# Kernel tuning notes

Hardware: AMD Instinct MI355X
Metric: run time of the kernel (lower is better)

Reference implementation:

```python
import jax, jax.numpy as jnp
import numpy as np

E = 8            # num_experts
K = 2            # top-k
CF = 1.25        # capacity_factor
NOISE_STD = 1.0 / E   # noise_mult / num_experts


def setup_inputs() -> dict:
    key = jax.random.key(0)
    ks = jax.random.split(key, 4)
    B, S, D, H = 8, 1024, 768, 3072
    x = jax.random.normal(ks[0], (B, S, D), jnp.float32)
    router_w = jax.random.normal(ks[1], (D, E), jnp.float32) * 0.02
    fc1_w = jax.random.normal(ks[2], (E, D, H), jnp.float32) * 0.02
    fc1_b = jnp.zeros((E, H), jnp.float32)
    fc2_w = jax.random.normal(ks[3], (E, H, D), jnp.float32) * 0.02
    fc2_b = jnp.zeros((E, D), jnp.float32)
    return dict(x=x, router_w=router_w, fc1_w=fc1_w, fc1_b=fc1_b, fc2_w=fc2_w, fc2_b=fc2_b)


def reference(x, router_w, fc1_w, fc1_b, fc2_w, fc2_b):
    B, S, D = x.shape
    N = B * S
    A = N * K                                   # total (token, slot) assignments
    capacity = int(round(K * N * CF / E))
    x_flat = x.reshape(N, D)

    # ---- router (eval mode: no noise, no dropout) ----
    logits = (x_flat @ router_w).astype(jnp.float32)          # [N,E]
    clean_probs = jax.nn.softmax(logits, axis=-1)
    noisy_logits = logits
    noisy_probs = jax.nn.softmax(noisy_logits, axis=-1)
    topk_probs, topk_idx = jax.lax.top_k(noisy_probs, K)      # [N,K]
    topk_probs = topk_probs.astype(x.dtype)

    flat_e = topk_idx.reshape(-1)                             # [A]
    expert_counts = jax.ops.segment_sum(jnp.ones((A,), jnp.float32), flat_e, num_segments=E)

    # ---- aux losses ----
    importance = clean_probs.sum(0)
    mi = importance.mean()
    loss_importance = jnp.var(importance) / (mi * mi + 1e-6)
    # kthvalue(noisy_logits, E-K+1) == (E-K+1)-th smallest == sorted[:, E-K]
    threshold = jnp.sort(noisy_logits, axis=-1)[:, E - K][:, None]
    prob_selected = 1.0 - jax.scipy.stats.norm.cdf(threshold - logits, loc=0.0, scale=NOISE_STD)
    load = prob_selected.sum(0)
    ml = load.mean()
    loss_load = jnp.var(load) / (ml * ml + 1e-6)
    aux_loss = 0.5 * (loss_importance + loss_load)

    # ---- priority-based capacity dropping (vectorized over all assignments) ----
    priority = clean_probs.max(-1)                            # [N]
    tok = jnp.repeat(jnp.arange(N, dtype=jnp.int32), K)       # [A] token of each assignment
    kslot = jnp.tile(jnp.arange(K, dtype=jnp.int32), N)       # [A] which top-k slot
    score = priority[tok] - kslot.astype(jnp.float32)         # combined_scores = -k_idx + priority
    # group by expert (ascending), within expert sort by score descending
    sort_key = flat_e.astype(jnp.float32) * (K + 2) - score
    order = jnp.argsort(sort_key)
    e_sorted = flat_e[order]
    counts = jax.ops.segment_sum(jnp.ones((A,), jnp.int32), flat_e, num_segments=E)
    starts = jnp.cumsum(counts) - counts
    rank_sorted = jnp.arange(A, dtype=jnp.int32) - starts[e_sorted]   # position within expert group
    rank = jnp.zeros((A,), jnp.int32).at[order].set(rank_sorted)
    keep = rank < capacity
    dropped = jnp.sum(~keep).astype(jnp.int32)

    # ---- dispatch into fixed [E, capacity] buffer (overflow slot sliced off) ----
    pos = jnp.where(keep, flat_e * capacity + rank, E * capacity)
    dispatch_tok = jnp.zeros((E * capacity + 1,), jnp.int32).at[pos].set(tok)[:-1]
    w_flat = topk_probs.reshape(-1)
    weight_buf = jnp.zeros((E * capacity + 1,), x.dtype).at[pos].set(jnp.where(keep, w_flat, 0.0))[:-1]

    xe = x_flat[dispatch_tok].reshape(E, capacity, D)         # gather
    h = jax.nn.gelu(jnp.einsum('ecd,edh->ech', xe, fc1_w) + fc1_b[:, None, :], approximate=False)
    ye = jnp.einsum('ech,ehd->ecd', h, fc2_w) + fc2_b[:, None, :]
    weighted = ye * weight_buf.reshape(E, capacity, 1)
    # padded slots have weight 0 and token 0 -> contribute nothing
    out_flat = jnp.zeros((N, D), x.dtype).at[dispatch_tok].add(weighted.reshape(E * capacity, D))

    return out_flat.reshape(B, S, D), aux_loss, dropped, expert_counts
```

## Files before the change

### kernel.cpp

```cpp
#include <hip/hip_runtime.h>
#include <hip/hip_bf16.h>
#include <math.h>

#define NTOK 8192
#define DIM  768
#define HDIM 3072
#define NE   8
#define CAP  2560
#define AMAX 16384

typedef __bf16 bf16x8  __attribute__((ext_vector_type(8)));
typedef __bf16 bf16x2  __attribute__((ext_vector_type(2)));
typedef float  floatx4 __attribute__((ext_vector_type(4)));

typedef unsigned int u32_g __attribute__((address_space(1)));
typedef unsigned int u32_l __attribute__((address_space(3)));

__device__ __forceinline__ void gl_lds16(const void* g, void* l) {
  __builtin_amdgcn_global_load_lds((const u32_g*)g, (u32_l*)l, 16, 0, 0);
}

__device__ __forceinline__ float gelu_exact(float v) {
  float z = fabsf(v) * 0.7071067811865475f;
  float t = __builtin_amdgcn_rcpf(1.0f + 0.3275911f * z);
  float p = ((((1.061405429f * t - 1.453152027f) * t + 1.421413741f) * t
              - 0.284496736f) * t + 0.254829592f) * t;
  float e = 1.0f - p * __expf(-z * z);
  e = copysignf(e, v);
  return 0.5f * v * (1.0f + e);
}

__global__ __launch_bounds__(256) void transpose_conv2(
    const float* __restrict__ w1, const float* __restrict__ w2,
    __bf16* __restrict__ o1, __bf16* __restrict__ o2)
{
  const int which = blockIdx.z;
  const float* src = which ? w2 : w1;
  __bf16* dst = which ? o2 : o1;
  const int Kd = which ? HDIM : DIM;
  const int Nd = which ? DIM : HDIM;
  const int e = blockIdx.y;
  const int tilesK = Kd >> 6;
  const int bk = blockIdx.x % tilesK, bn = blockIdx.x / tilesK;
  __shared__ float T[64][65];
  const float* se = src + (size_t)e * Kd * Nd;
  const int k0 = bk * 64, n0 = bn * 64;
  const int tid = threadIdx.x;
#pragma unroll
  for (int it = 0; it < 16; ++it) {
    int flat = tid + it * 256;
    int kk = flat >> 6, nn = flat & 63;
    T[kk][nn] = se[(size_t)(k0 + kk) * Nd + n0 + nn];
  }
  __syncthreads();
  const int n = tid >> 2, kg = tid & 3;
  bf16x8 v0, v1;
#pragma unroll
  for (int q = 0; q < 8; ++q) v0[q] = (__bf16)T[kg * 16 + q][n];
#pragma unroll
  for (int q = 0; q < 8; ++q) v1[q] = (__bf16)T[kg * 16 + 8 + q][n];
  __bf16* de = dst + (size_t)e * Nd * Kd + (size_t)(n0 + n) * Kd + k0 + kg * 16;
  *(bf16x8*)(de) = v0;
  *(bf16x8*)(de + 8) = v1;
}

__global__ __launch_bounds__(256) void router_kernel(
    const float* __restrict__ x, const float* __restrict__ rw,
    int* __restrict__ list_len, double* __restrict__ imp, double* __restrict__ loadacc,
    int* __restrict__ aidx, float* __restrict__ keyarr, float* __restrict__ warr)
{
  __shared__ float Wl[NE * DIM];
  __shared__ int   lcount[NE], lbase[NE];
  __shared__ int   s_e[32][2], s_pos[32][2];
  __shared__ float s_key[32][2], s_w[32][2];
  const int tid = threadIdx.x;
  for (int i = tid; i < NE * DIM; i += 256) {
    int e = i / DIM, d = i - e * DIM;
    Wl[i] = rw[d * NE + e];
  }
  if (tid < NE) lcount[tid] = 0;
  __syncthreads();
  const int wave = tid >> 6, lane = tid & 63;
  double my_imp = 0.0, my_load = 0.0;

  for (int it = 0; it < 8; ++it) {
    const int t = wave * 8 + it;
    const int n = blockIdx.x * 32 + t;
    const float* xr = x + (size_t)n * DIM;
    float part[NE];
#pragma unroll
    for (int e = 0; e < NE; ++e) part[e] = 0.f;
#pragma unroll
    for (int c = 0; c < DIM / 64; ++c) {
      float xv = xr[c * 64 + lane];
#pragma unroll
      for (int e = 0; e < NE; ++e) part[e] += xv * Wl[e * DIM + c * 64 + lane];
    }
#pragma unroll
    for (int off = 32; off > 0; off >>= 1) {
#pragma unroll
      for (int e = 0; e < NE; ++e) part[e] += __shfl_xor(part[e], off);
    }
    int e0 = 0; float v0 = part[0];
#pragma unroll
    for (int e = 1; e < NE; ++e) if (part[e] > v0) { v0 = part[e]; e0 = e; }
    int e1 = -1; float v1 = -3.4e38f;
#pragma unroll
    for (int e = 0; e < NE; ++e) if (e != e0 && part[e] > v1) { v1 = part[e]; e1 = e; }

    float pexp[NE]; float s = 0.f;
#pragma unroll
    for (int e = 0; e < NE; ++e) { pexp[e] = expf(part[e] - v0); s += pexp[e]; }
    const float inv = 1.0f / s;
    const float pr = inv;
    float w1v = 0.f;
#pragma unroll
    for (int e = 0; e < NE; ++e) if (e == e1) w1v = pexp[e] * inv;

    float myl = 0.f, mypexp = 0.f;
#pragma unroll
    for (int e = 0; e < NE; ++e) if (lane == e) { myl = part[e]; mypexp = pexp[e]; }
    if (lane < NE) {
      my_imp  += (double)(mypexp * inv);
      my_load += (double)(0.5f * erfcf((v1 - myl) * 5.656854249492380f));
    }
    if (lane == 0) {
      int p0 = atomicAdd(&lcount[e0], 1);
      int p1 = atomicAdd(&lcount[e1], 1);
      s_e[t][0] = e0; s_pos[t][0] = p0;
      s_key[t][0] = (float)(e0 * 4) - pr;
      s_w[t][0] = pr;
      s_e[t][1] = e1; s_pos[t][1] = p1;
      s_key[t][1] = (float)(e1 * 4) - (pr - 1.0f);
      s_w[t][1] = w1v;
    }
  }
  __syncthreads();
  if (tid < NE) lbase[tid] = atomicAdd(&list_len[tid], lcount[tid]);
  __syncthreads();
  if (tid < 64) {
    const int t = tid >> 1, sl = tid & 1;
    const int e = s_e[t][sl];
    const int gp = lbase[e] + s_pos[t][sl];
    const int n = blockIdx.x * 32 + t;
    aidx[e * AMAX + gp]   = n * 2 + sl;
    keyarr[e * AMAX + gp] = s_key[t][sl];
    warr[e * AMAX + gp]   = s_w[t][sl];
  }
  if (lane < NE) {
    unsafeAtomicAdd(&imp[lane], my_imp);
    unsafeAtomicAdd(&loadacc[lane], my_load);
  }
}

__global__ __launch_bounds__(256) void compact_kernel(
    const int* __restrict__ list_len, const int* __restrict__ aidx,
    const float* __restrict__ keyarr, const float* __restrict__ warr,
    int* __restrict__ dtok, float* __restrict__ dw,
    const double* __restrict__ imp, const double* __restrict__ loadacc,
    float* __restrict__ out_scalars)
{
  __shared__ float sk[6144];
  __shared__ int   sa[6144];
  const int e = blockIdx.x, tid = threadIdx.x;
  const int C = list_len[e];
  if (C <= CAP) {
    for (int t = tid; t < C; t += 256) {
      int a = aidx[e * AMAX + t];
      dtok[e * CAP + t] = a >> 1;
      dw[e * CAP + t]   = warr[e * AMAX + t];
    }
  } else {
    const bool useL = (C <= 6144);
    if (useL) {
      for (int t = tid; t < C; t += 256) { sk[t] = keyarr[e*AMAX+t]; sa[t] = aidx[e*AMAX+t]; }
      __syncthreads();
    }
    for (int t = tid; t < C; t += 256) {
      float kt = keyarr[e*AMAX+t]; int at = aidx[e*AMAX+t];
      int r = 0;
      for (int u = 0; u < C; ++u) {
        float ku = useL ? sk[u] : keyarr[e*AMAX+u];
        int   au = useL ? sa[u] : aidx[e*AMAX+u];
        if (ku < kt || (ku == kt && au < at)) ++r;
      }
      if (r < CAP) { dtok[e*CAP + r] = at >> 1; dw[e*CAP + r] = warr[e*AMAX+t]; }
    }
  }
  if (e == 0 && tid == 0) {
    double mi = 0, ml = 0;
    for (int i = 0; i < NE; ++i) { mi += imp[i]; ml += loadacc[i]; }
    mi /= NE; ml /= NE;
    double vi = 0, vl = 0;
    for (int i = 0; i < NE; ++i) {
      double di = imp[i] - mi;     vi += di * di;
      double dl = loadacc[i] - ml; vl += dl * dl;
    }
    vi /= NE; vl /= NE;
    double li = vi / (mi * mi + 1e-6), ll = vl / (ml * ml + 1e-6);
    out_scalars[0] = (float)(0.5 * (li + ll));
    int drop = 0;
    for (int i = 0; i < NE; ++i) { int c2 = list_len[i]; if (c2 > CAP) drop += c2 - CAP; }
    out_scalars[1] = (float)drop;
    for (int i = 0; i < NE; ++i) out_scalars[2 + i] = (float)list_len[i];
  }
}

__global__ __launch_bounds__(256) void gather_kernel(
    const float* __restrict__ x, const int* __restrict__ dtok,
    const int* __restrict__ list_len, __bf16* __restrict__ Ag)
{
  const int row  = blockIdx.x * 4 + (threadIdx.x >> 6);
  const int lane = threadIdx.x & 63;
  const int e = row / CAP, slot = row - e * CAP;
  const int kept = min(list_len[e], CAP);
  __bf16* dst = Ag + (size_t)row * DIM;
  if (slot < kept) {
    const float* srcr = x + (size_t)dtok[e * CAP + slot] * DIM;
#pragma unroll
    for (int c = 0; c < DIM / 128; ++c) {
      float2 v = *(const float2*)(srcr + c * 128 + lane * 2);
      bf16x2 o; o[0] = (__bf16)v.x; o[1] = (__bf16)v.y;
      *(bf16x2*)(dst + c * 128 + lane * 2) = o;
    }
  } else {
    bf16x2 z; z[0] = (__bf16)0.f; z[1] = (__bf16)0.f;
#pragma unroll
    for (int c = 0; c < DIM / 128; ++c) *(bf16x2*)(dst + c * 128 + lane * 2) = z;
  }
}

template<int MODE>
__global__ __launch_bounds__(256, 2) void moe_gemm(
    const __bf16* __restrict__ Aall, const __bf16* __restrict__ BTall,
    const float* __restrict__ bias, __bf16* __restrict__ Hout,
    float* __restrict__ Out, const int* __restrict__ dtok, const float* __restrict__ dww,
    const int* __restrict__ list_len, int Kd, int Nd, int tilesM)
{
  const int i_blk = blockIdx.x;
  const int xcd = i_blk & 7, q = i_blk >> 3;
  const int e = xcd;
  const int tm = q % tilesM;
  int tn, ks, kbase, kIters;
  if (MODE == 0) {
    tn = q / tilesM; ks = 0; kbase = 0; kIters = Kd >> 5;
  } else {
    const int pr = q / tilesM;
    tn = pr % 3; ks = pr / 3; kbase = ks * (Kd >> 1); kIters = Kd >> 6;
  }

  const int kept = min(list_len[e], CAP);
  const int mUsed = (kept + 127) >> 7;
  if (tm >= mUsed) return;

  __shared__ __bf16 S[3][12288];

  const int tid = threadIdx.x, lane = tid & 63, wave = tid >> 6;
  const int wm = wave & 1, wn = wave >> 1;
  const int m0 = tm * 128, n0 = tn * 256;

  const __bf16* Ae = Aall + (size_t)e * CAP * Kd + kbase;
  const __bf16* Be = BTall + (size_t)e * Nd * Kd + kbase;

  const int lr = lane & 15, lc = (lane >> 4) * 8;
  const __bf16* gA[2]; const __bf16* gB[4];
  int sAo[2], sBo[4];
#pragma unroll
  for (int a = 0; a < 2; ++a) {
    const int g = wave * 2 + a;
    gA[a] = Ae + (size_t)(m0 + g * 16 + lr) * Kd + lc;
    sAo[a] = g * 512;
  }
#pragma unroll
  for (int b = 0; b < 4; ++b) {
    const int h = wave * 4 + b;
    gB[b] = Be + (size_t)(n0 + h * 16 + lr) * Kd + lc;
    sBo[b] = 4096 + h * 512;
  }

  floatx4 acc[4][8];
#pragma unroll
  for (int i = 0; i < 4; ++i)
#pragma unroll
    for (int j = 0; j < 8; ++j) acc[i][j] = (floatx4)0.f;

#define ISSUE(J, Bf)                                           \
  do {                                                         \
    const int _off = (J) * 32;                                 \
    gl_lds16(gA[0] + _off, &S[(Bf)][sAo[0]]);                  \
    gl_lds16(gA[1] + _off, &S[(Bf)][sAo[1]]);                  \
    gl_lds16(gB[0] + _off, &S[(Bf)][sBo[0]]);                  \
    gl_lds16(gB[1] + _off, &S[(Bf)][sBo[1]]);                  \
    gl_lds16(gB[2] + _off, &S[(Bf)][sBo[2]]);                  \
    gl_lds16(gB[3] + _off, &S[(Bf)][sBo[3]]);                  \
  } while (0)

  ISSUE(0, 0);
  ISSUE(1, 1);
  int cur = 0;
  for (int kt = 0; kt < kIters; ++kt) {
    if (kt < kIters - 1) __builtin_amdgcn_s_waitcnt(0x0F76);
    else                 __builtin_amdgcn_s_waitcnt(0x0F70);
    asm volatile("" ::: "memory");
    __builtin_amdgcn_s_barrier();
    asm volatile("" ::: "memory");

    bf16x8 af[4], bfr[8];
#pragma unroll
    for (int i = 0; i < 4; ++i)
      af[i]  = *(const bf16x8*)(&S[cur][((wm * 4 + i) * 64 + lane) * 8]);
#pragma unroll
    for (int j = 0; j < 8; ++j)
      bfr[j] = *(const bf16x8*)(&S[cur][4096 + ((wn * 8 + j) * 64 + lane) * 8]);

    if (kt + 2 < kIters) {
      int nb = cur + 2; if (nb >= 3) nb -= 3;
      ISSUE(kt + 2, nb);
    }

#pragma unroll
    for (int i = 0; i < 4; ++i)
#pragma unroll
      for (int j = 0; j < 8; ++j)
        acc[i][j] = __builtin_amdgcn_mfma_f32_16x16x32_bf16(af[i], bfr[j], acc[i][j], 0, 0, 0);

    cur = (cur == 2) ? 0 : cur + 1;
  }
#undef ISSUE

  const int quad = lane >> 4, lcol = lane & 15;
  float bcol[8];
#pragma unroll
  for (int j = 0; j < 8; ++j)
    bcol[j] = (MODE == 1 && ks == 1) ? 0.f : bias[e * Nd + n0 + wn * 128 + j * 16 + lcol];

  if (MODE == 0) {
#pragma unroll
    for (int i = 0; i < 4; ++i) {
#pragma unroll
      for (int r = 0; r < 4; ++r) {
        const int row = m0 + wm * 64 + i * 16 + quad * 4 + r;
        __bf16* hrow = Hout + ((size_t)(e * CAP + row)) * Nd;
#pragma unroll
        for (int j = 0; j < 8; ++j) {
          float v = acc[i][j][r] + bcol[j];
          hrow[n0 + wn * 128 + j * 16 + lcol] = (__bf16)gelu_exact(v);
        }
      }
    }
  } else {
#pragma unroll
    for (int i = 0; i < 4; ++i) {
#pragma unroll
      for (int r = 0; r < 4; ++r) {
        const int row = m0 + wm * 64 + i * 16 + quad * 4 + r;
        const float w = dww[e * CAP + row];
        if (w != 0.0f) {
          const int tok = dtok[e * CAP + row];
          float* orow = Out + (size_t)tok * DIM;
#pragma unroll
          for (int j = 0; j < 8; ++j) {
            float v = w * (acc[i][j][r] + bcol[j]);
            unsafeAtomicAdd(&orow[n0 + wn * 128 + j * 16 + lcol], v);
          }
        }
      }
    }
  }
}

extern "C" void kernel_launch(void* const* d_in, const int* in_sizes, int n_in,
                              void* d_out, int out_size, void* d_ws, size_t ws_size,
                              hipStream_t stream) {
  (void)in_sizes; (void)n_in; (void)out_size; (void)ws_size;
  const float* x  = (const float*)d_in[0];
  const float* rw = (const float*)d_in[1];
  const float* w1 = (const float*)d_in[2];
  const float* b1 = (const float*)d_in[3];
  const float* w2 = (const float*)d_in[4];
  const float* b2 = (const float*)d_in[5];
  float* out = (float*)d_out;
  char* ws = (char*)d_ws;

  int*    list_len = (int*)(ws + 0);
  double* imp      = (double*)(ws + 64);
  double* loadacc  = (double*)(ws + 128);
  int*    dtok     = (int*)(ws + 256);
  float*  dw       = (float*)(ws + 256 + 81920);
  int*    aidx     = (int*)(ws + 164096);
  float*  keyarr   = (float*)(ws + 164096 + 524288);
  float*  warr     = (float*)(ws + 164096 + 1048576);
  __bf16* W1T      = (__bf16*)(ws + 2097152);
  __bf16* W2T      = (__bf16*)(ws + 2097152 + 37748736);
  __bf16* Ag       = (__bf16*)(ws + 2097152 + 2 * 37748736);
  __bf16* hbuf     = (__bf16*)(ws + 2097152 + 2 * 37748736 + 31457280);

  hipMemsetAsync(d_out, 0, (size_t)NTOK * DIM * sizeof(float), stream);
  hipMemsetAsync(ws, 0, 164096, stream);

  transpose_conv2<<<dim3(576, 8, 2), 256, 0, stream>>>(w1, w2, W1T, W2T);
  router_kernel<<<NTOK / 32, 256, 0, stream>>>(x, rw, list_len, imp, loadacc, aidx, keyarr, warr);
  compact_kernel<<<NE, 256, 0, stream>>>(list_len, aidx, keyarr, warr, dtok, dw, imp, loadacc,
                                         out + (size_t)NTOK * DIM);
  gather_kernel<<<(NE * CAP) / 4, 256, 0, stream>>>(x, dtok, list_len, Ag);
  moe_gemm<0><<<NE * 20 * (HDIM / 256), 256, 0, stream>>>(
      Ag, W1T, b1, hbuf, nullptr, nullptr, nullptr, list_len, DIM, HDIM, 20);
  moe_gemm<1><<<NE * 20 * (DIM / 256) * 2, 256, 0, stream>>>(
      hbuf, W2T, b2, nullptr, out, dtok, dw, list_len, HDIM, DIM, 20);
}
```

Before: 577.8 us.

## Restructure MoE GEMMs into 256x256 tiles with 8-wave ping-pong pipeline

Replaces the 128x256 tile, 4-wave, triple-buffered GEMM with a 256x256 tile, 8-wave (512-thread) kernel. It uses two 64-wide K stages in LDS and interleaves quarter-tile LDS reads, global-to-LDS loads and MFMA blocks, separated by barriers and s_setprio. The second GEMM drops its split-K in favour of the full K loop, which halves its atomic adds but launches fewer blocks. The goal is higher arithmetic intensity per block and better overlap of loads with MFMA. The cost is 128 KB of LDS per block, more barriers, and less parallelism for the small-N second GEMM.

Result: faster. 549.0 us (-5.0%).

```diff
diff --git a/kernel.cpp b/kernel.cpp
--- a/kernel.cpp
+++ b/kernel.cpp
@@ -230,144 +230,185 @@
   }
 }
 
+#define BAR() do { asm volatile("" ::: "memory"); __builtin_amdgcn_s_barrier(); asm volatile("" ::: "memory"); } while (0)
+
+#define ST_A(h, t, buf) do { \
+    const __bf16* _g = gA[h] + (size_t)(t) * 64; \
+    gl_lds16(_g,      &S[buf][((h) * 8 + wave) * 1024]); \
+    gl_lds16(_g + 32, &S[buf][((h) * 8 + wave) * 1024 + 512]); \
+  } while (0)
+
+#define ST_B(h, t, buf) do { \
+    const __bf16* _g = gB[h] + (size_t)(t) * 64; \
+    gl_lds16(_g,      &S[buf][16384 + ((h) * 8 + wave) * 1024]); \
+    gl_lds16(_g + 32, &S[buf][16384 + ((h) * 8 + wave) * 1024 + 512]); \
+  } while (0)
+
+#define RD_A(qm, buf) do { \
+    _Pragma("unroll") \
+    for (int _m = 0; _m < 4; ++_m) { \
+      const int _g = wm * 8 + (qm) * 4 + _m; \
+      aR[_m][0] = *(const bf16x8*)&S[buf][(_g * 2 + 0) * 512 + lane * 8]; \
+      aR[_m][1] = *(const bf16x8*)&S[buf][(_g * 2 + 1) * 512 + lane * 8]; \
+    } \
+  } while (0)
+
+#define RD_B(qn, buf) do { \
+    _Pragma("unroll") \
+    for (int _n = 0; _n < 2; ++_n) { \
+      const int _g = wn * 4 + (qn) * 2 + _n; \
+      bR[(qn) * 2 + _n][0] = *(const bf16x8*)&S[buf][16384 + (_g * 2 + 0) * 512 + lane * 8]; \
+      bR[(qn) * 2 + _n][1] = *(const bf16x8*)&S[buf][16384 + (_g * 2 + 1) * 512 + lane * 8]; \
+    } \
+  } while (0)
+
+#define MM(qm, qn) do { \
+    __builtin_amdgcn_s_setprio(1); \
+    _Pragma("unroll") \
+    for (int _m = 0; _m < 4; ++_m) \
+      _Pragma("unroll") \
+      for (int _n = 0; _n < 2; ++_n) { \
+        acc[(qm) * 4 + _m][(qn) * 2 + _n] = __builtin_amdgcn_mfma_f32_16x16x32_bf16( \
+            aR[_m][0], bR[(qn) * 2 + _n][0], acc[(qm) * 4 + _m][(qn) * 2 + _n], 0, 0, 0); \
+        acc[(qm) * 4 + _m][(qn) * 2 + _n] = __builtin_amdgcn_mfma_f32_16x16x32_bf16( \
+            aR[_m][1], bR[(qn) * 2 + _n][1], acc[(qm) * 4 + _m][(qn) * 2 + _n], 0, 0, 0); \
+      } \
+    __builtin_amdgcn_s_setprio(0); \
+  } while (0)
+
 template<int MODE>
-__global__ __launch_bounds__(256, 2) void moe_gemm(
+__global__ __launch_bounds__(512, 2) void moe_gemm8(
     const __bf16* __restrict__ Aall, const __bf16* __restrict__ BTall,
     const float* __restrict__ bias, __bf16* __restrict__ Hout,
     float* __restrict__ Out, const int* __restrict__ dtok, const float* __restrict__ dww,
-    const int* __restrict__ list_len, int Kd, int Nd, int tilesM)
+    const int* __restrict__ list_len)
 {
+  const int Kd = MODE ? HDIM : DIM;
+  const int Nd = MODE ? DIM : HDIM;
+  const int numKt = Kd / 64;
+  const int nIter = numKt / 2;
+
   const int i_blk = blockIdx.x;
-  const int xcd = i_blk & 7, q = i_blk >> 3;
-  const int e = xcd;
-  const int tm = q % tilesM;
-  int tn, ks, kbase, kIters;
-  if (MODE == 0) {
-    tn = q / tilesM; ks = 0; kbase = 0; kIters = Kd >> 5;
-  } else {
-    const int pr = q / tilesM;
-    tn = pr % 3; ks = pr / 3; kbase = ks * (Kd >> 1); kIters = Kd >> 6;
-  }
+  const int e = i_blk & 7;
+  const int q = i_blk >> 3;
+  const int tm = q % 10, tn = q / 10;
 
   const int kept = min(list_len[e], CAP);
-  const int mUsed = (kept + 127) >> 7;
-  if (tm >= mUsed) return;
-
-  __shared__ __bf16 S[3][12288];
+  if (tm >= ((kept + 255) >> 8)) return;
+
+  __shared__ __align__(16) __bf16 S[2][32768];
 
   const int tid = threadIdx.x, lane = tid & 63, wave = tid >> 6;
   const int wm = wave & 1, wn = wave >> 1;
-  const int m0 = tm * 128, n0 = tn * 256;
-
-  const __bf16* Ae = Aall + (size_t)e * CAP * Kd + kbase;
-  const __bf16* Be = BTall + (size_t)e * Nd * Kd + kbase;
-
-  const int lr = lane & 15, lc = (lane >> 4) * 8;
-  const __bf16* gA[2]; const __bf16* gB[4];
-  int sAo[2], sBo[4];
-#pragma unroll
-  for (int a = 0; a < 2; ++a) {
-    const int g = wave * 2 + a;
-    gA[a] = Ae + (size_t)(m0 + g * 16 + lr) * Kd + lc;
-    sAo[a] = g * 512;
-  }
-#pragma unroll
-  for (int b = 0; b < 4; ++b) {
-    const int h = wave * 4 + b;
-    gB[b] = Be + (size_t)(n0 + h * 16 + lr) * Kd + lc;
-    sBo[b] = 4096 + h * 512;
-  }
-
-  floatx4 acc[4][8];
-#pragma unroll
-  for (int i = 0; i < 4; ++i)
-#pragma unroll
-    for (int j = 0; j < 8; ++j) acc[i][j] = (floatx4)0.f;
-
-#define ISSUE(J, Bf)                                           \
-  do {                                                         \
-    const int _off = (J) * 32;                                 \
-    gl_lds16(gA[0] + _off, &S[(Bf)][sAo[0]]);                  \
-    gl_lds16(gA[1] + _off, &S[(Bf)][sAo[1]]);                  \
-    gl_lds16(gB[0] + _off, &S[(Bf)][sBo[0]]);                  \
-    gl_lds16(gB[1] + _off, &S[(Bf)][sBo[1]]);                  \
-    gl_lds16(gB[2] + _off, &S[(Bf)][sBo[2]]);                  \
-    gl_lds16(gB[3] + _off, &S[(Bf)][sBo[3]]);                  \
-  } while (0)
-
-  ISSUE(0, 0);
-  ISSUE(1, 1);
-  int cur = 0;
-  for (int kt = 0; kt < kIters; ++kt) {
-    if (kt < kIters - 1) __builtin_amdgcn_s_waitcnt(0x0F76);
-    else                 __builtin_amdgcn_s_waitcnt(0x0F70);
-    asm volatile("" ::: "memory");
-    __builtin_amdgcn_s_barrier();
-    asm volatile("" ::: "memory");
-
-    bf16x8 af[4], bfr[8];
-#pragma unroll
-    for (int i = 0; i < 4; ++i)
-      af[i]  = *(const bf16x8*)(&S[cur][((wm * 4 + i) * 64 + lane) * 8]);
-#pragma unroll
-    for (int j = 0; j < 8; ++j)
-      bfr[j] = *(const bf16x8*)(&S[cur][4096 + ((wn * 8 + j) * 64 + lane) * 8]);
-
-    if (kt + 2 < kIters) {
-      int nb = cur + 2; if (nb >= 3) nb -= 3;
-      ISSUE(kt + 2, nb);
-    }
-
-#pragma unroll
-    for (int i = 0; i < 4; ++i)
-#pragma unroll
-      for (int j = 0; j < 8; ++j)
-        acc[i][j] = __builtin_amdgcn_mfma_f32_16x16x32_bf16(af[i], bfr[j], acc[i][j], 0, 0, 0);
-
-    cur = (cur == 2) ? 0 : cur + 1;
-  }
-#undef ISSUE
+  const int m0 = tm * 256, n0 = tn * 256;
+  const int lr = lane & 15, kq = lane >> 4;
+
+  const __bf16* Abase = Aall + (size_t)e * CAP * Kd;
+  const __bf16* Bbase = BTall + (size_t)e * Nd * Kd;
+
+  const __bf16* gA[2]; const __bf16* gB[2];
+#pragma unroll
+  for (int h = 0; h < 2; ++h) {
+    gA[h] = Abase + (size_t)(m0 + (h * 8 + wave) * 16 + lr) * Kd + kq * 8;
+    gB[h] = Bbase + (size_t)(n0 + (h * 8 + wave) * 16 + lr) * Kd + kq * 8;
+  }
+
+  floatx4 acc[8][4];
+#pragma unroll
+  for (int i = 0; i < 8; ++i)
+#pragma unroll
+    for (int j = 0; j < 4; ++j) acc[i][j] = (floatx4)0.f;
+
+  bf16x8 aR[4][2], bR[4][2];
+
+  ST_A(0, 0, 0); ST_A(1, 0, 0); ST_B(0, 0, 0); ST_B(1, 0, 0);
+  ST_A(0, 1, 1);
+  __builtin_amdgcn_s_waitcnt(0x0F72);
+  BAR();
+
+#pragma unroll 1
+  for (int i = 0; i < nIter; ++i) {
+    const int t0 = 2 * i;
+    const bool more = (i < nIter - 1);
+
+    RD_A(0, 0); RD_B(0, 0);
+    ST_A(1, t0 + 1, 1);
+    BAR(); MM(0, 0); BAR();
+    RD_B(1, 0);
+    ST_B(0, t0 + 1, 1);
+    BAR(); MM(0, 1); BAR();
+    RD_A(1, 0);
+    ST_B(1, t0 + 1, 1);
+    BAR(); MM(1, 1); BAR();
+    if (more) {
+      ST_A(0, t0 + 2, 0);
+      __builtin_amdgcn_s_waitcnt(0x0F72);
+    } else {
+      __builtin_amdgcn_s_waitcnt(0x0F70);
+    }
+    BAR(); MM(1, 0); BAR();
+
+    RD_A(0, 1); RD_B(0, 1);
+    if (more) ST_A(1, t0 + 2, 0);
+    BAR(); MM(0, 0); BAR();
+    RD_B(1, 1);
+    if (more) ST_B(0, t0 + 2, 0);
+    BAR(); MM(0, 1); BAR();
+    RD_A(1, 1);
+    if (more) ST_B(1, t0 + 2, 0);
+    BAR(); MM(1, 1); BAR();
+    if (more) {
+      ST_A(0, t0 + 3, 1);
+      __builtin_amdgcn_s_waitcnt(0x0F72);
+    } else {
+      __builtin_amdgcn_s_waitcnt(0x0F70);
+    }
+    BAR(); MM(1, 0); BAR();
+  }
 
   const int quad = lane >> 4, lcol = lane & 15;
-  float bcol[8];
-#pragma unroll
-  for (int j = 0; j < 8; ++j)
-    bcol[j] = (MODE == 1 && ks == 1) ? 0.f : bias[e * Nd + n0 + wn * 128 + j * 16 + lcol];
+  float bcol[4];
+#pragma unroll
+  for (int n = 0; n < 4; ++n)
+    bcol[n] = bias[e * Nd + n0 + wn * 64 + n * 16 + lcol];
 
   if (MODE == 0) {
 #pragma unroll
-    for (int i = 0; i < 4; ++i) {
+    for (int m = 0; m < 8; ++m) {
 #pragma unroll
       for (int r = 0; r < 4; ++r) {
-        const int row = m0 + wm * 64 + i * 16 + quad * 4 + r;
-        __bf16* hrow = Hout + ((size_t)(e * CAP + row)) * Nd;
-#pragma unroll
-        for (int j = 0; j < 8; ++j) {
-          float v = acc[i][j][r] + bcol[j];
-          hrow[n0 + wn * 128 + j * 16 + lcol] = (__bf16)gelu_exact(v);
-        }
+        const int row = m0 + wm * 128 + m * 16 + quad * 4 + r;
+        __bf16* hrow = Hout + ((size_t)(e * CAP + row)) * Nd + n0 + wn * 64;
+#pragma unroll
+        for (int n = 0; n < 4; ++n)
+          hrow[n * 16 + lcol] = (__bf16)gelu_exact(acc[m][n][r] + bcol[n]);
       }
     }
   } else {
 #pragma unroll
-    for (int i = 0; i < 4; ++i) {
+    for (int m = 0; m < 8; ++m) {
 #pragma unroll
       for (int r = 0; r < 4; ++r) {
-        const int row = m0 + wm * 64 + i * 16 + quad * 4 + r;
+        const int row = m0 + wm * 128 + m * 16 + quad * 4 + r;
         const float w = dww[e * CAP + row];
         if (w != 0.0f) {
           const int tok = dtok[e * CAP + row];
-          float* orow = Out + (size_t)tok * DIM;
-#pragma unroll
-          for (int j = 0; j < 8; ++j) {
-            float v = w * (acc[i][j][r] + bcol[j]);
-            unsafeAtomicAdd(&orow[n0 + wn * 128 + j * 16 + lcol], v);
-          }
+          float* orow = Out + (size_t)tok * DIM + n0 + wn * 64;
+#pragma unroll
+          for (int n = 0; n < 4; ++n)
+            unsafeAtomicAdd(&orow[n * 16 + lcol], w * (acc[m][n][r] + bcol[n]));
         }
       }
     }
   }
 }
+
+#undef BAR
+#undef ST_A
+#undef ST_B
+#undef RD_A
+#undef RD_B
+#undef MM
 
 extern "C" void kernel_launch(void* const* d_in, const int* in_sizes, int n_in,
                               void* d_out, int out_size, void* d_ws, size_t ws_size,
@@ -403,8 +444,8 @@
   compact_kernel<<<NE, 256, 0, stream>>>(list_len, aidx, keyarr, warr, dtok, dw, imp, loadacc,
                                          out + (size_t)NTOK * DIM);
   gather_kernel<<<(NE * CAP) / 4, 256, 0, stream>>>(x, dtok, list_len, Ag);
-  moe_gemm<0><<<NE * 20 * (HDIM / 256), 256, 0, stream>>>(
-      Ag, W1T, b1, hbuf, nullptr, nullptr, nullptr, list_len, DIM, HDIM, 20);
-  moe_gemm<1><<<NE * 20 * (DIM / 256) * 2, 256, 0, stream>>>(
-      hbuf, W2T, b2, nullptr, out, dtok, dw, list_len, HDIM, DIM, 20);
-}
+  moe_gemm8<0><<<NE * 10 * (HDIM / 256), 512, 0, stream>>>(
+      Ag, W1T, b1, hbuf, nullptr, nullptr, nullptr, list_len);
+  moe_gemm8<1><<<NE * 10 * (DIM / 256), 512, 0, stream>>>(
+      hbuf, W2T, b2, nullptr, out, dtok, dw, list_len);
+}
```
